# Kernel tuning notes

Hardware: AMD Instinct MI355X
Metric: run time of the kernel (lower is better)

The kernel has to match this reference:

```python
import jax, jax.numpy as jnp
import numpy as np
from jax.scipy.linalg import solve_triangular


def setup_inputs() -> dict:
    key = jax.random.key(0)
    k1, k2 = jax.random.split(key)
    # [K classes, N per class, D features] training embeddings
    src_seq = jax.random.normal(k1, (256, 64, 128), dtype=jnp.float32)
    # [M, D] vectors to project and pairwise-score (clustering inner loop)
    test = jax.random.normal(k2, (8192, 128), dtype=jnp.float32)
    return {"src_seq": src_seq, "test": test}


def _fit_model(src_seq):
    # Faithful port of compute_scatter_matrices + fit_model.
    # S_w, S_b are symmetric PSD, so solve(S_w,S_b) eig is replaced by the
    # equivalent (and differentiable) generalized symmetric eig via Cholesky
    # whitening; A_inverse and psi are invariant to eigvec scaling/order.
    K, N, D = src_seq.shape
    count = K * N
    mean_per_class = src_seq.mean(axis=1)            # [K, D]
    mean = src_seq.mean(axis=(0, 1))                 # [D]
    diff_w = src_seq - mean_per_class[:, None, :]    # [K, N, D]
    diff_b = mean_per_class - mean                   # [K, D]
    S_w = jnp.einsum('knd,kne->de', diff_w, diff_w) / count   # [D, D]
    S_b = (N * jnp.einsum('kd,ke->de', diff_b, diff_b)) / count

    L = jnp.linalg.cholesky(S_w)                     # S_w = L L^T
    # Msym = L^{-1} S_b L^{-T}
    tmp = solve_triangular(L, S_b, lower=True)
    Msym = solve_triangular(L, tmp.T, lower=True).T
    Msym = 0.5 * (Msym + Msym.T)
    evals, U = jnp.linalg.eigh(Msym)
    W = solve_triangular(L, U, lower=True, trans=1)  # W = L^{-T} U, eigvecs of S_w^{-1} S_b

    lambda_b = jnp.sum(W * (S_b @ W), axis=0)        # diag(W^T S_b W)
    lambda_w = jnp.sum(W * (S_w @ W), axis=0)        # diag(W^T S_w W)
    n = float(N)
    # A = W^{-T} diag(sqrt(n/(n-1) * lambda_w))  =>  A^{-1} = diag(1/sqrt(.)) W^T
    A_inverse = (1.0 / jnp.sqrt(n / (n - 1.0) * lambda_w))[:, None] * W.T
    psi = jnp.clip((n - 1.0) / n * (lambda_b / lambda_w) - 1.0 / n, 0.0)
    return A_inverse, mean, psi


def reference(src_seq, test):
    A_inverse, mean, psi = _fit_model(src_seq)
    # latent = A_inverse @ (x - mean), batched over rows
    latent = (test - mean) @ A_inverse.T             # [M, D]
    # Pairwise single-vector probability (calculate_probability_single),
    # vectorized over all (i, j) pairs, in log space:
    # log p(i,j) = -(v_i - v_j)^T diag(psi) (v_i - v_j)
    #             - 0.5 * (D*log(2*pi) + log(||psi||_F))
    D = latent.shape[1]
    q = jnp.sum(psi * latent * latent, axis=1)       # [M]
    G = (latent * psi) @ latent.T                    # [M, M]
    maha = q[:, None] + q[None, :] - 2.0 * G         # [M, M]
    log_div = 0.5 * (D * jnp.log(2.0 * jnp.pi) + jnp.log(jnp.linalg.norm(psi)))
    return -maha - log_div                           # [M, M] pairwise log-prob
```

## Files before the change

### kernel.cpp

```cpp
#include <hip/hip_runtime.h>
#include <math.h>


#define D 128
#define NCLS 256
#define NPC 64
#define MTEST 8192
#define COUNT (NCLS*NPC)

#define fMC    0
#define fMEAN  16384
#define fSCAL  16640
#define fMAT   32768
#define fSWRAW 442368
#define fPART  458752
#define fU     458752
#define fV     983040
#define fQ     1507328
#define fBBF   1515520

#define sP   0
#define sSB  1
#define sP2  2
#define sP3  3
#define sP4  4
#define sZ   5
#define sM1  6
#define sMm  7
#define sC2  8
#define sC4  9
#define sXH  10
#define sT2  11
#define sT3  12
#define sT4  13
#define sT5  14
#define sT10 15
#define sT15 16
#define sT20 17
#define sG0  18
#define sF   23
#define sA1  24

using short8 = __attribute__((ext_vector_type(8))) short;
using f32x4  = __attribute__((ext_vector_type(4))) float;

__device__ inline unsigned short f2bf(float f) {
  unsigned u = __float_as_uint(f);
  unsigned r = u + 0x7FFFu + ((u >> 16) & 1u);
  return (unsigned short)(r >> 16);
}
__device__ inline float bf2f(unsigned short h) {
  return __uint_as_float(((unsigned)h) << 16);
}
__device__ inline float valU(const unsigned short* m, int idx) {
  return bf2f(m[idx]) + bf2f(m[idx + 16384]);
}
__device__ inline void storeDual(unsigned short* m, int idx, float g) {
  unsigned short hb = f2bf(g);
  m[idx] = hb;
  m[16384 + idx] = f2bf(g - bf2f(hb));
}
__device__ inline unsigned short* MS(float* ws, int m) {
  return (unsigned short*)(ws + fMAT) + (size_t)m * 32768;
}
__device__ inline const unsigned short* MSc(const float* ws, int m) {
  return (const unsigned short*)(ws + fMAT) + (size_t)m * 32768;
}

__global__ __launch_bounds__(256) void k_gt_partial(const float* __restrict__ X, float* __restrict__ ws) {
  __shared__ unsigned short xt[128 * 256];
  int b = blockIdx.x, tid = threadIdx.x;
  const float* Xc = X + b * 256 * D;
  for (int idx = tid; idx < 256 * D; idx += 256) {
    int s = idx >> 7, d = idx & 127;
    unsigned byte = ((unsigned)(d * 512 + s * 2)) ^ (((unsigned)(d & 7)) << 4);
    *(unsigned short*)((char*)xt + byte) = f2bf(Xc[idx]);
  }
  {
    int d = tid & 127;
    for (int cc = (tid >> 7); cc < 4; cc += 2) {
      const float* p = Xc + cc * 64 * D + d;
      float s = 0.f;
      #pragma unroll
      for (int n = 0; n < 64; n++) s += p[n * D];
      ((unsigned short*)ws)[d * 256 + (b * 4 + cc)] = f2bf(s * (1.0f / 64.0f));
    }
  }
  __syncthreads();
  int w = tid >> 6, lane = tid & 63;
  int wr = (w >> 1) * 64, wc = (w & 1) * 64;
  f32x4 acc[4][4] = {};
  for (int ks = 0; ks < 8; ks++) {
    int kb = ks * 32 + (lane >> 4) * 8;
    short8 af[4];
    #pragma unroll
    for (int mt = 0; mt < 4; mt++) {
      int r = wr + mt * 16 + (lane & 15);
      unsigned byte = ((unsigned)(r * 512 + kb * 2)) ^ (((unsigned)(r & 7)) << 4);
      af[mt] = *(short8*)((char*)xt + byte);
    }
    #pragma unroll
    for (int nt = 0; nt < 4; nt++) {
      int c = wc + nt * 16 + (lane & 15);
      unsigned byte = ((unsigned)(c * 512 + kb * 2)) ^ (((unsigned)(c & 7)) << 4);
      short8 bfr = *(short8*)((char*)xt + byte);
      #pragma unroll
      for (int mt = 0; mt < 4; mt++)
        acc[mt][nt] = __builtin_amdgcn_mfma_f32_16x16x32_bf16(af[mt], bfr, acc[mt][nt], 0, 0, 0);
    }
  }
  float* outp = ws + fPART + b * 16384;
  #pragma unroll
  for (int mt = 0; mt < 4; mt++)
    #pragma unroll
    for (int nt = 0; nt < 4; nt++)
      #pragma unroll
      for (int r = 0; r < 4; r++) {
        int row = wr + mt * 16 + (lane >> 4) * 4 + r;
        int col = wc + nt * 16 + (lane & 15);
        outp[row * 128 + col] = acc[mt][nt][r];
      }
}

__global__ void k_reduce(float* __restrict__ ws) {
  int tid = threadIdx.x;
  int idx = blockIdx.x * 256 + tid;
  const float* part = ws + fPART;
  float s = 0.f;
  #pragma unroll 8
  for (int p = 0; p < 64; p++) s += part[p * 16384 + idx];
  ws[fSWRAW + idx] = s;
  if (blockIdx.x == 0 && tid < 128) {
    const unsigned short* McT = (const unsigned short*)ws;
    float m = 0.f;
    for (int k = 0; k < 256; k++) m += bf2f(McT[tid * 256 + k]);
    ws[fMEAN + tid] = m * (1.0f / 256.0f);
  }
}

__global__ __launch_bounds__(256) void k_sb(float* __restrict__ ws) {
  __shared__ float red[4];
  const unsigned short* Mc = (const unsigned short*)ws;
  const float* mv = ws + fMEAN;
  const float* swraw = ws + fSWRAW;
  unsigned short* SB = MS(ws, sSB);
  float* scal = ws + fSCAL;
  int tid = threadIdx.x, b = blockIdx.x;
  int w = tid >> 6, lane = tid & 63;
  int brow = b * 32, wcol = w * 32;
  f32x4 acc[2][2] = {};
  for (int ks = 0; ks < 8; ks++) {
    int kb = ks * 32 + (lane >> 4) * 8;
    short8 af[2], bfv[2];
    #pragma unroll
    for (int mt = 0; mt < 2; mt++) {
      int r = brow + mt * 16 + (lane & 15);
      af[mt] = *(const short8*)(Mc + r * 256 + kb);
    }
    #pragma unroll
    for (int nt = 0; nt < 2; nt++) {
      int c = wcol + nt * 16 + (lane & 15);
      bfv[nt] = *(const short8*)(Mc + c * 256 + kb);
    }
    #pragma unroll
    for (int mt = 0; mt < 2; mt++)
      #pragma unroll
      for (int nt = 0; nt < 2; nt++)
        acc[mt][nt] = __builtin_amdgcn_mfma_f32_16x16x32_bf16(af[mt], bfv[nt], acc[mt][nt], 0, 0, 0);
  }
  float tsum = 0.f;
  #pragma unroll
  for (int mt = 0; mt < 2; mt++)
    #pragma unroll
    for (int nt = 0; nt < 2; nt++)
      #pragma unroll
      for (int r = 0; r < 4; r++) {
        int row = brow + mt * 16 + (lane >> 4) * 4 + r;
        int col = wcol + nt * 16 + (lane & 15);
        int idx = row * 128 + col;
        float g = acc[mt][nt][r] * (1.0f / 256.0f) - mv[row] * mv[col];
        storeDual(SB, idx, g);
        if (row == col)
          tsum += swraw[row * 129] * (1.0f / COUNT) - g - mv[row] * mv[row];
      }
  #pragma unroll
  for (int off = 32; off > 0; off >>= 1) tsum += __shfl_down(tsum, off);
  if (lane == 0) red[w] = tsum;
  __syncthreads();
  if (tid == 0) scal[64 + b] = red[0] + red[1] + red[2] + red[3];
}

__global__ __launch_bounds__(256) void k_swfin(float* __restrict__ ws) {
  float* scal = ws + fSCAL;
  float inv_s = 128.0f / (scal[64] + scal[65] + scal[66] + scal[67]);
  const float* mv = ws + fMEAN;
  const float* swraw = ws + fSWRAW;
  const unsigned short* SB = MS(ws, sSB);
  unsigned short* P = MS(ws, sP);
  int gid = blockIdx.x * 256 + threadIdx.x;
  #pragma unroll
  for (int t = 0; t < 4; t++) {
    int idx = gid * 4 + t;
    int row = idx >> 7, col = idx & 127;
    float sb = valU(SB, idx);
    float s = (swraw[idx] * (1.0f / COUNT) - sb - mv[row] * mv[col]) * inv_s;
    storeDual(P, idx, s - ((row == col) ? 1.0f : 0.0f));
  }
  if (blockIdx.x == 0 && threadIdx.x == 0) {
    scal[1] = inv_s;
    scal[7] = 0.984375f * inv_s;
  }
}

__device__ __forceinline__ void mm_body(
    const unsigned short* __restrict__ A, const unsigned short* __restrict__ B,
    unsigned short* __restrict__ C, const unsigned short* __restrict__ E1,
    float alpha, const float* alpha_ptr, float beta, float delta,
    float* scal, int trace_slot, unsigned short* outBf, int b, float* red) {
  int tid = threadIdx.x;
  int w = tid >> 6, lane = tid & 63;
  int brow = b * 32, wcol = w * 32;
  f32x4 acc[2][2] = {};
  #pragma unroll
  for (int ks = 0; ks < 4; ks++) {
    int kb = ks * 32 + (lane >> 4) * 8;
    short8 ah[2], al[2], bh[2], bl[2];
    #pragma unroll
    for (int mt = 0; mt < 2; mt++) {
      int r = brow + mt * 16 + (lane & 15);
      ah[mt] = *(const short8*)(A + r * 128 + kb);
      al[mt] = *(const short8*)(A + 16384 + r * 128 + kb);
    }
    #pragma unroll
    for (int nt = 0; nt < 2; nt++) {
      int c = wcol + nt * 16 + (lane & 15);
      bh[nt] = *(const short8*)(B + c * 128 + kb);
      bl[nt] = *(const short8*)(B + 16384 + c * 128 + kb);
    }
    #pragma unroll
    for (int mt = 0; mt < 2; mt++)
      #pragma unroll
      for (int nt = 0; nt < 2; nt++) {
        f32x4 a0 = acc[mt][nt];
        a0 = __builtin_amdgcn_mfma_f32_16x16x32_bf16(ah[mt], bh[nt], a0, 0, 0, 0);
        a0 = __builtin_amdgcn_mfma_f32_16x16x32_bf16(al[mt], bh[nt], a0, 0, 0, 0);
        a0 = __builtin_amdgcn_mfma_f32_16x16x32_bf16(ah[mt], bl[nt], a0, 0, 0, 0);
        acc[mt][nt] = a0;
      }
  }
  float aeff = alpha * (alpha_ptr ? alpha_ptr[0] : 1.0f);
  float tsum = 0.0f;
  #pragma unroll
  for (int mt = 0; mt < 2; mt++)
    #pragma unroll
    for (int nt = 0; nt < 2; nt++)
      #pragma unroll
      for (int r = 0; r < 4; r++) {
        int row = brow + mt * 16 + (lane >> 4) * 4 + r;
        int col = wcol + nt * 16 + (lane & 15);
        int idx = row * 128 + col;
        float g = acc[mt][nt][r] * aeff;
        if (E1) g += beta * (bf2f(E1[idx]) + bf2f(E1[16384 + idx]));
        if (row == col) g += delta;
        if (outBf) outBf[idx] = f2bf(g);
        else storeDual(C, idx, g);
        tsum += g * g;
      }
  if (trace_slot >= 0) {
    #pragma unroll
    for (int off = 32; off > 0; off >>= 1) tsum += __shfl_down(tsum, off);
    if (lane == 0) red[w] = tsum;
    __syncthreads();
    if (tid == 0) scal[trace_slot + b] = red[0] + red[1] + red[2] + red[3];
  }
}

__global__ __launch_bounds__(256) void k_mm(
    const unsigned short* A, const unsigned short* B, unsigned short* C,
    const unsigned short* E1, float alpha, const float* alpha_ptr,
    float beta, float delta, float* scal, int trace_slot, unsigned short* outBf) {
  __shared__ float red[4];
  mm_body(A, B, C, E1, alpha, alpha_ptr, beta, delta, scal, trace_slot, outBf, blockIdx.x, red);
}

__global__ __launch_bounds__(256) void k_mm2(
    const unsigned short* A0, const unsigned short* B0, unsigned short* C0,
    const unsigned short* E0, float al0, float be0, float de0,
    const unsigned short* A1, const unsigned short* B1, unsigned short* C1,
    const unsigned short* E1, float al1, float be1, float de1,
    float* scal, int tslot1) {
  __shared__ float red[4];
  int b = blockIdx.x & 3;
  if (blockIdx.x < 4)
    mm_body(A0, B0, C0, E0, al0, nullptr, be0, de0, scal, -1, nullptr, b, red);
  else
    mm_body(A1, B1, C1, E1, al1, nullptr, be1, de1, scal, tslot1, nullptr, b, red);
}

__global__ __launch_bounds__(256) void k_p56z(float* __restrict__ ws) {
  __shared__ float cj[7];
  __shared__ float bt[7];
  float* scal = ws + fSCAL;
  const unsigned short *P = MSc(ws, sP), *P2 = MSc(ws, sP2),
    *P3 = MSc(ws, sP3), *P4 = MSc(ws, sP4);
  unsigned short* Z = MS(ws, sZ);
  int tid = threadIdx.x, b = blockIdx.x;
  float trP8 = scal[60] + scal[61] + scal[62] + scal[63];
  float a = 1.05f * sqrtf(sqrtf(sqrtf(fmaxf(trP8, 1e-30f))));
  a = fminf(a, 0.95f);
  if (tid < 7) {
    const float PI = 3.14159265358979f;
    float s = 0.f;
    for (int i = 0; i < 64; i++) {
      float th = (i + 0.5f) * (PI / 64.0f);
      float x = cosf(th);
      s += (1.0f / sqrtf(1.0f + a * x)) * cosf((float)tid * th);
    }
    cj[tid] = s * (2.0f / 64.0f);
  }
  __syncthreads();
  if (tid == 0) {
    float c0h = 0.5f * cj[0];
    float m0 = c0h - cj[2] + cj[4] - cj[6];
    float m1 = cj[1] - 3.0f * cj[3] + 5.0f * cj[5];
    float m2 = 2.0f * cj[2] - 8.0f * cj[4] + 18.0f * cj[6];
    float m3 = 4.0f * cj[3] - 20.0f * cj[5];
    float m4 = 8.0f * cj[4] - 48.0f * cj[6];
    float m5 = 16.0f * cj[5];
    float m6 = 32.0f * cj[6];
    float ia = 1.0f / a;
    float p = 1.f;
    bt[0] = m0;
    p *= ia; bt[1] = m1 * p;
    p *= ia; bt[2] = m2 * p;
    p *= ia; bt[3] = m3 * p;
    p *= ia; bt[4] = m4 * p;
    p *= ia; bt[5] = m5 * p;
    p *= ia; bt[6] = m6 * p;
  }
  __syncthreads();
  int w = tid >> 6, lane = tid & 63;
  int brow = b * 32, wcol = w * 32;
  f32x4 a5[2][2] = {}, a6[2][2] = {};
  #pragma unroll
  for (int ks = 0; ks < 4; ks++) {
    int kb = ks * 32 + (lane >> 4) * 8;
    short8 ah[2], al[2], b5h[2], b5l[2], b6h[2], b6l[2];
    #pragma unroll
    for (int mt = 0; mt < 2; mt++) {
      int r = brow + mt * 16 + (lane & 15);
      ah[mt] = *(const short8*)(P4 + r * 128 + kb);
      al[mt] = *(const short8*)(P4 + 16384 + r * 128 + kb);
    }
    #pragma unroll
    for (int nt = 0; nt < 2; nt++) {
      int c = wcol + nt * 16 + (lane & 15);
      b5h[nt] = *(const short8*)(P + c * 128 + kb);
      b5l[nt] = *(const short8*)(P + 16384 + c * 128 + kb);
      b6h[nt] = *(const short8*)(P2 + c * 128 + kb);
      b6l[nt] = *(const short8*)(P2 + 16384 + c * 128 + kb);
    }
    #pragma unroll
    for (int mt = 0; mt < 2; mt++)
      #pragma unroll
      for (int nt = 0; nt < 2; nt++) {
        f32x4 x5 = a5[mt][nt];
        x5 = __builtin_amdgcn_mfma_f32_16x16x32_bf16(ah[mt], b5h[nt], x5, 0, 0, 0);
        x5 = __builtin_amdgcn_mfma_f32_16x16x32_bf16(al[mt], b5h[nt], x5, 0, 0, 0);
        x5 = __builtin_amdgcn_mfma_f32_16x16x32_bf16(ah[mt], b5l[nt], x5, 0, 0, 0);
        a5[mt][nt] = x5;
        f32x4 x6 = a6[mt][nt];
        x6 = __builtin_amdgcn_mfma_f32_16x16x32_bf16(ah[mt], b6h[nt], x6, 0, 0, 0);
        x6 = __builtin_amdgcn_mfma_f32_16x16x32_bf16(al[mt], b6h[nt], x6, 0, 0, 0);
        x6 = __builtin_amdgcn_mfma_f32_16x16x32_bf16(ah[mt], b6l[nt], x6, 0, 0, 0);
        a6[mt][nt] = x6;
      }
  }
  #pragma unroll
  for (int mt = 0; mt < 2; mt++)
    #pragma unroll
    for (int nt = 0; nt < 2; nt++)
      #pragma unroll
      for (int r = 0; r < 4; r++) {
        int row = brow + mt * 16 + (lane >> 4) * 4 + r;
        int col = wcol + nt * 16 + (lane & 15);
        int idx = row * 128 + col;
        float dg = (row == col) ? 1.0f : 0.0f;
        float z = bt[0] * dg + bt[1] * valU(P, idx) + bt[2] * valU(P2, idx) +
                  bt[3] * valU(P3, idx) + bt[4] * valU(P4, idx) +
                  bt[5] * a5[mt][nt][r] + bt[6] * a6[mt][nt][r];
        storeDual(Z, idx, z);
      }
}

__device__ inline void interval_cs(const float* scal, float* c0o, float* iho) {
  float trM8 = scal[68] + scal[69] + scal[70] + scal[71];
  float Lam = 1.03f * sqrtf(sqrtf(sqrtf(fmaxf(trM8, 1e-37f))));
  float lo = -0.02f * Lam, hi = Lam;
  *c0o = 0.5f * (hi + lo);
  *iho = 1.0f / (0.5f * (hi - lo));
}

__global__ __launch_bounds__(256) void k_xh_t2(float* __restrict__ ws) {
  __shared__ float cs[2];
  float* scal = ws + fSCAL;
  if (threadIdx.x == 0) {
    float c0, ih;
    interval_cs(scal, &c0, &ih);
    cs[0] = c0; cs[1] = ih;
  }
  __syncthreads();
  float c0 = cs[0], ih = cs[1];
  float a2 = 2.0f * ih * ih, b2 = -4.0f * c0 * ih * ih, g2 = 2.0f * c0 * c0 * ih * ih - 1.0f;
  const unsigned short* Mm = MSc(ws, sMm);
  const unsigned short* C2 = MSc(ws, sC2);
  unsigned short* XH = MS(ws, sXH);
  unsigned short* T2 = MS(ws, sT2);
  int gid = blockIdx.x * 256 + threadIdx.x;
  #pragma unroll
  for (int t = 0; t < 4; t++) {
    int idx = gid * 4 + t;
    int row = idx >> 7, col = idx & 127;
    float m = valU(Mm, idx), c2v = valU(C2, idx);
    float dg = (row == col) ? 1.0f : 0.0f;
    storeDual(XH, idx, ih * m - ih * c0 * dg);
    storeDual(T2, idx, a2 * c2v + b2 * m + g2 * dg);
  }
}

__global__ __launch_bounds__(256) void k_t5g(float* __restrict__ ws) {
  __shared__ float red[4];
  __shared__ float cs[8];
  __shared__ float sat[25];
  __shared__ float sc[25];
  float* scal = ws + fSCAL;
  int tid = threadIdx.x;
  if (blockIdx.x < 4) {
    mm_body(MSc(ws, sT2), MSc(ws, sT3), MS(ws, sT5), MSc(ws, sXH),
            2.0f, nullptr, -1.0f, 0.0f, scal, -1, nullptr, blockIdx.x, red);
    return;
  }
  if (tid == 0) {
    float c0, ih;
    interval_cs(scal, &c0, &ih);
    float inv_s = scal[1];
    float t0 = (1.0f / 63.0f) / inv_s;
    float x0 = fminf(fmaxf((t0 - c0) * ih, -1.0f), 1.0f);
    cs[0] = acosf(x0); cs[1] = x0;
    cs[2] = 0.984375f * inv_s / ih;
  }
  __syncthreads();
  if (tid <= 24) {
    float th = cs[0], x0 = cs[1], SCc = cs[2];
    const float PI = 3.14159265358979f;
    float v;
    if (tid == 0) v = 0.5f * SCc * (2.0f / PI) * (sinf(th) - x0 * th);
    else if (tid == 1) v = SCc * (2.0f / PI) * (0.5f * th + 0.25f * sinf(2.0f * th) - x0 * sinf(th));
    else {
      float fj = (float)tid;
      v = SCc * (2.0f / PI) *
          (0.5f * (sinf((fj + 1.0f) * th) / (fj + 1.0f) + sinf((fj - 1.0f) * th) / (fj - 1.0f))
           - x0 * sinf(fj * th) / fj);
    }
    sat[tid] = v;
    sc[tid] = 0.f;
  }
  __syncthreads();
  if (tid == 0) {
    for (int j = 24; j >= 5; --j) {
      int k = j / 5, r = j - 5 * k;
      float aj = sat[j];
      if (r == 0) sc[k * 5] += aj;
      else { sc[k * 5 + r] += 2.0f * aj; sat[5 * k - r] -= aj; }
    }
    for (int r = 0; r < 5; r++) sc[r] += sat[r];
  }
  __syncthreads();
  const unsigned short* XH = MSc(ws, sXH);
  const unsigned short* T2 = MSc(ws, sT2);
  const unsigned short* T3 = MSc(ws, sT3);
  const unsigned short* T4 = MSc(ws, sT4);
  int bg = blockIdx.x - 4;
  int base = bg * 1024 + tid * 4;
  #pragma unroll
  for (int t = 0; t < 4; t++) {
    int idx = base + t;
    int row = idx >> 7, col = idx & 127;
    float dg = (row == col) ? 1.0f : 0.0f;
    float x1 = valU(XH, idx), x2 = valU(T2, idx), x3 = valU(T3, idx), x4 = valU(T4, idx);
    #pragma unroll
    for (int k = 0; k < 5; k++) {
      float g = sc[k * 5 + 0] * dg + sc[k * 5 + 1] * x1 + sc[k * 5 + 2] * x2 +
                sc[k * 5 + 3] * x3 + sc[k * 5 + 4] * x4;
      storeDual(MS(ws, sG0 + k), idx, g);
    }
  }
}

__global__ __launch_bounds__(256) void k_bigF(float* __restrict__ ws) {
  __shared__ float red[4];
  float* scal = ws + fSCAL;
  const unsigned short* As[4] = { MSc(ws, sT5), MSc(ws, sT10), MSc(ws, sT15), MSc(ws, sT20) };
  const unsigned short* Bs[4] = { MSc(ws, sG0 + 1), MSc(ws, sG0 + 2), MSc(ws, sG0 + 3), MSc(ws, sG0 + 4) };
  const unsigned short* G0 = MSc(ws, sG0);
  unsigned short* Fm = MS(ws, sF);
  int tid = threadIdx.x, b = blockIdx.x;
  int w = tid >> 6, lane = tid & 63;
  int brow = b * 32, wcol = w * 32;
  f32x4 acc[2][2] = {};
  for (int p = 0; p < 4; p++) {
    const unsigned short* A = As[p];
    const unsigned short* B = Bs[p];
    #pragma unroll
    for (int ks = 0; ks < 4; ks++) {
      int kb = ks * 32 + (lane >> 4) * 8;
      short8 ah[2], al[2], bh[2], bl[2];
      #pragma unroll
      for (int mt = 0; mt < 2; mt++) {
        int r = brow + mt * 16 + (lane & 15);
        ah[mt] = *(const short8*)(A + r * 128 + kb);
        al[mt] = *(const short8*)(A + 16384 + r * 128 + kb);
      }
      #pragma unroll
      for (int nt = 0; nt < 2; nt++) {
        int c = wcol + nt * 16 + (lane & 15);
        bh[nt] = *(const short8*)(B + c * 128 + kb);
        bl[nt] = *(const short8*)(B + 16384 + c * 128 + kb);
      }
      #pragma unroll
      for (int mt = 0; mt < 2; mt++)
        #pragma unroll
        for (int nt = 0; nt < 2; nt++) {
          f32x4 a0 = acc[mt][nt];
          a0 = __builtin_amdgcn_mfma_f32_16x16x32_bf16(ah[mt], bh[nt], a0, 0, 0, 0);
          a0 = __builtin_amdgcn_mfma_f32_16x16x32_bf16(al[mt], bh[nt], a0, 0, 0, 0);
          a0 = __builtin_amdgcn_mfma_f32_16x16x32_bf16(ah[mt], bl[nt], a0, 0, 0, 0);
          acc[mt][nt] = a0;
        }
    }
  }
  float tsum = 0.f;
  #pragma unroll
  for (int mt = 0; mt < 2; mt++)
    #pragma unroll
    for (int nt = 0; nt < 2; nt++)
      #pragma unroll
      for (int r = 0; r < 4; r++) {
        int row = brow + mt * 16 + (lane >> 4) * 4 + r;
        int col = wcol + nt * 16 + (lane & 15);
        int idx = row * 128 + col;
        float g = acc[mt][nt][r] + valU(G0, idx);
        storeDual(Fm, idx, g);
        tsum += g * g;
      }
  #pragma unroll
  for (int off = 32; off > 0; off >>= 1) tsum += __shfl_down(tsum, off);
  if (lane == 0) red[w] = tsum;
  __syncthreads();
  if (tid == 0) scal[72 + b] = red[0] + red[1] + red[2] + red[3];
}

__global__ __launch_bounds__(256) void k_latent(const float* __restrict__ test, float* __restrict__ ws) {
  __shared__ unsigned short vh[16384];
  __shared__ float qs[128];
  int blk = blockIdx.x, tid = threadIdx.x;
  if (blk == 0 && tid == 0) {
    float* scal = ws + fSCAL;
    float trF2 = fmaxf(scal[72] + scal[73] + scal[74] + scal[75], 1e-30f);
    scal[0] = 0.5f * (128.0f * 1.8378770664093453f + 0.5f * logf(trF2));
  }
  const float* tb = test + blk * 128 * D;
  unsigned short* Vbf = (unsigned short*)(ws + fV);
  if (tid < 128) qs[tid] = 0.f;
  for (int idx = tid; idx < 16384; idx += 256) {
    int r = idx >> 7, c = idx & 127;
    float v = tb[idx] - ws[fMEAN + c];
    unsigned short h = f2bf(v);
    unsigned byte = ((unsigned)(r * 256 + c * 2)) ^ (((unsigned)(r & 7)) << 4);
    *(unsigned short*)((char*)vh + byte) = h;
    Vbf[blk * 16384 + idx] = h;
  }
  __syncthreads();
  int w = tid >> 6, lane = tid & 63;
  int wr = (w >> 1) * 64, wc = (w & 1) * 64;
  const unsigned short* Bbf = (const unsigned short*)(ws + fBBF);
  f32x4 acc[4][4] = {};
  for (int ks = 0; ks < 4; ks++) {
    int kb = ks * 32 + (lane >> 4) * 8;
    short8 af[4], bfv[4];
    #pragma unroll
    for (int mt = 0; mt < 4; mt++) {
      int r = wr + mt * 16 + (lane & 15);
      unsigned byte = ((unsigned)(r * 256 + kb * 2)) ^ (((unsigned)(r & 7)) << 4);
      af[mt] = *(short8*)((char*)vh + byte);
    }
    #pragma unroll
    for (int nt = 0; nt < 4; nt++) {
      int c = wc + nt * 16 + (lane & 15);
      bfv[nt] = *(const short8*)(Bbf + c * 128 + kb);
    }
    #pragma unroll
    for (int mt = 0; mt < 4; mt++)
      #pragma unroll
      for (int nt = 0; nt < 4; nt++)
        acc[mt][nt] = __builtin_amdgcn_mfma_f32_16x16x32_bf16(af[mt], bfv[nt], acc[mt][nt], 0, 0, 0);
  }
  unsigned short* Ubf = (unsigned short*)(ws + fU);
  #pragma unroll
  for (int mt = 0; mt < 4; mt++)
    #pragma unroll
    for (int nt = 0; nt < 4; nt++)
      #pragma unroll
      for (int r = 0; r < 4; r++) {
        int row = wr + mt * 16 + (lane >> 4) * 4 + r;
        int col = wc + nt * 16 + (lane & 15);
        Ubf[(blk * 128 + row) * 128 + col] = f2bf(acc[mt][nt][r]);
      }
  #pragma unroll
  for (int mt = 0; mt < 4; mt++)
    #pragma unroll
    for (int r = 0; r < 4; r++) {
      int row = wr + mt * 16 + (lane >> 4) * 4 + r;
      float p = 0.f;
      #pragma unroll
      for (int nt = 0; nt < 4; nt++) {
        int col = wc + nt * 16 + (lane & 15);
        unsigned byte = ((unsigned)(row * 256 + col * 2)) ^ (((unsigned)(row & 7)) << 4);
        p += bf2f(f2bf(acc[mt][nt][r])) * bf2f(*(unsigned short*)((char*)vh + byte));
      }
      p += __shfl_xor(p, 1, 16);
      p += __shfl_xor(p, 2, 16);
      p += __shfl_xor(p, 4, 16);
      p += __shfl_xor(p, 8, 16);
      if ((lane & 15) == 0) atomicAdd(&qs[row], p);
    }
  __syncthreads();
  if (tid < 128) ws[fQ + blk * 128 + tid] = qs[tid];
}

__global__ __launch_bounds__(256) void k_pair(const float* __restrict__ ws, float* __restrict__ out) {
  __shared__ float qi[128];
  __shared__ float qj[128];
  __shared__ float sld;
  int bi = blockIdx.x, bj = blockIdx.y, tid = threadIdx.x;
  if (tid < 128) qi[tid] = ws[fQ + bi * 128 + tid];
  else qj[tid - 128] = ws[fQ + bj * 128 + (tid - 128)];
  if (tid == 0) sld = ws[fSCAL + 0];
  __syncthreads();
  int w = tid >> 6, lane = tid & 63;
  int wr = (w >> 1) * 64, wc = (w & 1) * 64;
  const unsigned short* Ubf = (const unsigned short*)(ws + fU);
  const unsigned short* Vbf = (const unsigned short*)(ws + fV);
  f32x4 acc[4][4] = {};
  for (int ks = 0; ks < 4; ks++) {
    int kb = ks * 32 + (lane >> 4) * 8;
    short8 af[4], bfv[4];
    #pragma unroll
    for (int mt = 0; mt < 4; mt++) {
      int r = bi * 128 + wr + mt * 16 + (lane & 15);
      af[mt] = *(const short8*)(Ubf + r * 128 + kb);
    }
    #pragma unroll
    for (int nt = 0; nt < 4; nt++) {
      int c = bj * 128 + wc + nt * 16 + (lane & 15);
      bfv[nt] = *(const short8*)(Vbf + c * 128 + kb);
    }
    #pragma unroll
    for (int mt = 0; mt < 4; mt++)
      #pragma unroll
      for (int nt = 0; nt < 4; nt++)
        acc[mt][nt] = __builtin_amdgcn_mfma_f32_16x16x32_bf16(af[mt], bfv[nt], acc[mt][nt], 0, 0, 0);
  }
  float ld = sld;
  #pragma unroll
  for (int mt = 0; mt < 4; mt++)
    #pragma unroll
    for (int nt = 0; nt < 4; nt++)
      #pragma unroll
      for (int r = 0; r < 4; r++) {
        int row = wr + mt * 16 + (lane >> 4) * 4 + r;
        int col = wc + nt * 16 + (lane & 15);
        float g = acc[mt][nt][r];
        out[(size_t)(bi * 128 + row) * MTEST + (bj * 128 + col)] =
          2.0f * g - qi[row] - qj[col] - ld;
      }
}

extern "C" void kernel_launch(void* const* d_in, const int* in_sizes, int n_in,
                              void* d_out, int out_size, void* d_ws, size_t ws_size,
                              hipStream_t stream) {
  (void)in_sizes; (void)n_in; (void)out_size; (void)ws_size;
  const float* X = (const float*)d_in[0];
  const float* test = (const float*)d_in[1];
  float* out = (float*)d_out;
  float* ws = (float*)d_ws;
  float* scal = ws + fSCAL;
  auto M = [&](int i) -> unsigned short* {
    return (unsigned short*)(ws + fMAT) + (size_t)i * 32768;
  };
  unsigned short* Bbf = (unsigned short*)(ws + fBBF);

  k_gt_partial<<<64, 256, 0, stream>>>(X, ws);
  k_reduce<<<64, 256, 0, stream>>>(ws);
  k_sb<<<4, 256, 0, stream>>>(ws);
  k_swfin<<<16, 256, 0, stream>>>(ws);
  k_mm<<<4, 256, 0, stream>>>(M(sP), M(sP), M(sP2), nullptr, 1.0f, nullptr, 0, 0, scal, -1, nullptr);
  k_mm2<<<8, 256, 0, stream>>>(M(sP2), M(sP), M(sP3), nullptr, 1.0f, 0, 0,
                               M(sP2), M(sP2), M(sP4), nullptr, 1.0f, 0, 0, scal, 60);
  k_p56z<<<4, 256, 0, stream>>>(ws);
  k_mm<<<4, 256, 0, stream>>>(M(sZ), M(sSB), M(sM1), nullptr, 1.0f, nullptr, 0, 0, scal, -1, nullptr);
  k_mm<<<4, 256, 0, stream>>>(M(sM1), M(sZ), M(sMm), nullptr, 1.0f, nullptr, 0, 0, scal, -1, nullptr);
  k_mm<<<4, 256, 0, stream>>>(M(sMm), M(sMm), M(sC2), nullptr, 1.0f, nullptr, 0, 0, scal, -1, nullptr);
  k_mm<<<4, 256, 0, stream>>>(M(sC2), M(sC2), M(sC4), nullptr, 1.0f, nullptr, 0, 0, scal, 68, nullptr);
  k_xh_t2<<<16, 256, 0, stream>>>(ws);
  k_mm2<<<8, 256, 0, stream>>>(M(sXH), M(sT2), M(sT3), M(sXH), 2.0f, -1.0f, 0,
                               M(sT2), M(sT2), M(sT4), nullptr, 2.0f, 0, -1.0f, scal, -1);
  k_t5g<<<20, 256, 0, stream>>>(ws);
  k_mm<<<4, 256, 0, stream>>>(M(sT5), M(sT5), M(sT10), nullptr, 2.0f, nullptr, 0, -1.0f, scal, -1, nullptr);
  k_mm2<<<8, 256, 0, stream>>>(M(sT10), M(sT5), M(sT15), M(sT5), 2.0f, -1.0f, 0,
                               M(sT10), M(sT10), M(sT20), nullptr, 2.0f, 0, -1.0f, scal, -1);
  k_bigF<<<4, 256, 0, stream>>>(ws);
  k_mm<<<4, 256, 0, stream>>>(M(sZ), M(sF), M(sA1), nullptr, 1.0f, nullptr, 0, 0, scal, -1, nullptr);
  k_mm<<<4, 256, 0, stream>>>(M(sA1), M(sZ), nullptr, nullptr, 1.0f, scal + 7, 0, 0, scal, -1, Bbf);
  k_latent<<<64, 256, 0, stream>>>(test, ws);
  k_pair<<<dim3(64, 64), 256, 0, stream>>>(ws, out);
}
```

Measured before the change: 277.8 us.

## Fuse matrix-function chain into fewer kernels with LDS-chained products

Cuts the serial chain of small 128x128 split-bf16 matmul launches from about 19 to about 13. It fuses S_b and P construction, computes the P^2/P^3/P^4 chain within a block using LDS-resident row tiles, and moves the test-minus-mean conversion into spare blocks of the powers kernel. It also lowers the polynomial/Chebyshev degrees (7-term to 5-term, T20 to T16 style), switches to 1024-thread blocks with one 16x16 tile per wave, and computes the S_w trace scale in the reduce kernel. The goal is less launch and dependency latency in the tiny sequential prologue before the large pairwise kernel. The lower approximation degree risks accuracy.

```diff
diff --git a/kernel.cpp b/kernel.cpp
--- a/kernel.cpp
+++ b/kernel.cpp
@@ -25,21 +25,17 @@
 #define sP3  3
 #define sP4  4
 #define sZ   5
-#define sM1  6
 #define sMm  7
 #define sC2  8
-#define sC4  9
 #define sXH  10
 #define sT2  11
 #define sT3  12
 #define sT4  13
-#define sT5  14
-#define sT10 15
-#define sT15 16
-#define sT20 17
+#define sT8  14
+#define sT12 15
+#define sT16 16
 #define sG0  18
 #define sF   23
-#define sA1  24
 
 using short8 = __attribute__((ext_vector_type(8))) short;
 using f32x4  = __attribute__((ext_vector_type(4))) float;
@@ -63,8 +59,52 @@
 __device__ inline unsigned short* MS(float* ws, int m) {
   return (unsigned short*)(ws + fMAT) + (size_t)m * 32768;
 }
-__device__ inline const unsigned short* MSc(const float* ws, int m) {
-  return (const unsigned short*)(ws + fMAT) + (size_t)m * 32768;
+__device__ inline short8 st8(const unsigned short* L, int rloc, int colk) {
+  unsigned u = ((unsigned)(rloc * 128 + colk)) ^ (((unsigned)(rloc & 7)) << 3);
+  return *(const short8*)(L + u);
+}
+__device__ inline float stValU(const unsigned short* L, int rloc, int col) {
+  unsigned u = ((unsigned)(rloc * 128 + col)) ^ (((unsigned)(rloc & 7)) << 3);
+  return bf2f(L[u]) + bf2f(L[4096 + u]);
+}
+__device__ inline void stPutDual(unsigned short* L, int rloc, int col, float g) {
+  unsigned u = ((unsigned)(rloc * 128 + col)) ^ (((unsigned)(rloc & 7)) << 3);
+  unsigned short hb = f2bf(g);
+  L[u] = hb;
+  L[4096 + u] = f2bf(g - bf2f(hb));
+}
+
+__device__ __forceinline__ f32x4 tile_AB(const unsigned short* __restrict__ A, int rA,
+                                         const unsigned short* __restrict__ B, int cB,
+                                         int lane, f32x4 acc) {
+  #pragma unroll
+  for (int ks = 0; ks < 4; ks++) {
+    int kb = ks * 32 + (lane >> 4) * 8;
+    short8 ah = *(const short8*)(A + rA * 128 + kb);
+    short8 al = *(const short8*)(A + 16384 + rA * 128 + kb);
+    short8 bh = *(const short8*)(B + cB * 128 + kb);
+    short8 bl = *(const short8*)(B + 16384 + cB * 128 + kb);
+    acc = __builtin_amdgcn_mfma_f32_16x16x32_bf16(ah, bh, acc, 0, 0, 0);
+    acc = __builtin_amdgcn_mfma_f32_16x16x32_bf16(al, bh, acc, 0, 0, 0);
+    acc = __builtin_amdgcn_mfma_f32_16x16x32_bf16(ah, bl, acc, 0, 0, 0);
+  }
+  return acc;
+}
+__device__ __forceinline__ f32x4 tile_LB(const unsigned short* __restrict__ L, int rloc,
+                                         const unsigned short* __restrict__ B, int cB,
+                                         int lane, f32x4 acc) {
+  #pragma unroll
+  for (int ks = 0; ks < 4; ks++) {
+    int kb = ks * 32 + (lane >> 4) * 8;
+    short8 ah = st8(L, rloc, kb);
+    short8 al = st8(L + 4096, rloc, kb);
+    short8 bh = *(const short8*)(B + cB * 128 + kb);
+    short8 bl = *(const short8*)(B + 16384 + cB * 128 + kb);
+    acc = __builtin_amdgcn_mfma_f32_16x16x32_bf16(ah, bh, acc, 0, 0, 0);
+    acc = __builtin_amdgcn_mfma_f32_16x16x32_bf16(al, bh, acc, 0, 0, 0);
+    acc = __builtin_amdgcn_mfma_f32_16x16x32_bf16(ah, bl, acc, 0, 0, 0);
+  }
+  return acc;
 }
 
 __global__ __launch_bounds__(256) void k_gt_partial(const float* __restrict__ X, float* __restrict__ ws) {
@@ -123,6 +163,7 @@
 }
 
 __global__ void k_reduce(float* __restrict__ ws) {
+  __shared__ float red2[4];
   int tid = threadIdx.x;
   int idx = blockIdx.x * 256 + tid;
   const float* part = ws + fPART;
@@ -136,179 +177,139 @@
     for (int k = 0; k < 256; k++) m += bf2f(McT[tid * 256 + k]);
     ws[fMEAN + tid] = m * (1.0f / 256.0f);
   }
-}
-
-__global__ __launch_bounds__(256) void k_sb(float* __restrict__ ws) {
-  __shared__ float red[4];
+  if (blockIdx.x == 1) {
+    float v = 0.f;
+    if (tid < 128) {
+      float gdd = 0.f;
+      for (int p = 0; p < 64; p++) gdd += part[p * 16384 + tid * 129];
+      const unsigned short* McT = (const unsigned short*)ws;
+      float nrm = 0.f;
+      for (int k = 0; k < 256; k++) { float x = bf2f(McT[tid * 256 + k]); nrm += x * x; }
+      v = gdd * (1.0f / COUNT) - nrm * (1.0f / 256.0f);
+    }
+    #pragma unroll
+    for (int off = 32; off > 0; off >>= 1) v += __shfl_down(v, off);
+    if ((tid & 63) == 0) red2[tid >> 6] = v;
+    __syncthreads();
+    if (tid == 0) {
+      float inv_s = 128.0f / (red2[0] + red2[1] + red2[2] + red2[3]);
+      ws[fSCAL + 1] = inv_s;
+      ws[fSCAL + 7] = 0.984375f * inv_s;
+    }
+  }
+}
+
+__global__ __launch_bounds__(1024) void k_sbp(float* __restrict__ ws) {
   const unsigned short* Mc = (const unsigned short*)ws;
   const float* mv = ws + fMEAN;
   const float* swraw = ws + fSWRAW;
+  float inv_s = ws[fSCAL + 1];
   unsigned short* SB = MS(ws, sSB);
+  unsigned short* P = MS(ws, sP);
+  int tid = threadIdx.x, b = blockIdx.x;
+  int w = tid >> 6, lane = tid & 63;
+  int wr = (w & 1) * 16, wc = (w >> 1) * 16;
+  int brow = b * 32;
+  f32x4 acc = {};
+  for (int ks = 0; ks < 8; ks++) {
+    int kb = ks * 32 + (lane >> 4) * 8;
+    short8 af = *(const short8*)(Mc + (brow + wr + (lane & 15)) * 256 + kb);
+    short8 bf = *(const short8*)(Mc + (wc + (lane & 15)) * 256 + kb);
+    acc = __builtin_amdgcn_mfma_f32_16x16x32_bf16(af, bf, acc, 0, 0, 0);
+  }
+  #pragma unroll
+  for (int r = 0; r < 4; r++) {
+    int row = brow + wr + (lane >> 4) * 4 + r;
+    int col = wc + (lane & 15);
+    int idx = row * 128 + col;
+    float g = acc[r] * (1.0f / 256.0f) - mv[row] * mv[col];
+    storeDual(SB, idx, g);
+    float s = (swraw[idx] * (1.0f / COUNT) - g - mv[row] * mv[col]) * inv_s;
+    storeDual(P, idx, s - ((row == col) ? 1.0f : 0.0f));
+  }
+}
+
+__global__ __launch_bounds__(1024) void k_pows(const float* __restrict__ test, float* __restrict__ ws) {
+  __shared__ unsigned short sA[8192];
+  __shared__ unsigned short sB[8192];
+  __shared__ float red[16];
   float* scal = ws + fSCAL;
   int tid = threadIdx.x, b = blockIdx.x;
-  int w = tid >> 6, lane = tid & 63;
-  int brow = b * 32, wcol = w * 32;
-  f32x4 acc[2][2] = {};
-  for (int ks = 0; ks < 8; ks++) {
-    int kb = ks * 32 + (lane >> 4) * 8;
-    short8 af[2], bfv[2];
-    #pragma unroll
-    for (int mt = 0; mt < 2; mt++) {
-      int r = brow + mt * 16 + (lane & 15);
-      af[mt] = *(const short8*)(Mc + r * 256 + kb);
-    }
-    #pragma unroll
-    for (int nt = 0; nt < 2; nt++) {
-      int c = wcol + nt * 16 + (lane & 15);
-      bfv[nt] = *(const short8*)(Mc + c * 256 + kb);
-    }
-    #pragma unroll
-    for (int mt = 0; mt < 2; mt++)
-      #pragma unroll
-      for (int nt = 0; nt < 2; nt++)
-        acc[mt][nt] = __builtin_amdgcn_mfma_f32_16x16x32_bf16(af[mt], bfv[nt], acc[mt][nt], 0, 0, 0);
-  }
+  if (b >= 4) {
+    unsigned short* Vbf = (unsigned short*)(ws + fV);
+    const float* mv = ws + fMEAN;
+    int base = (b - 4) * 32768;
+    #pragma unroll 4
+    for (int k = 0; k < 32; k++) {
+      int idx = base + k * 1024 + tid;
+      Vbf[idx] = f2bf(test[idx] - mv[idx & 127]);
+    }
+    return;
+  }
+  const unsigned short* P = MS(ws, sP);
+  unsigned short* P2 = MS(ws, sP2);
+  unsigned short* P3 = MS(ws, sP3);
+  unsigned short* P4 = MS(ws, sP4);
+  int w = tid >> 6, lane = tid & 63;
+  int wr = (w & 1) * 16, wc = (w >> 1) * 16;
+  int brow = b * 32;
   float tsum = 0.f;
-  #pragma unroll
-  for (int mt = 0; mt < 2; mt++)
-    #pragma unroll
-    for (int nt = 0; nt < 2; nt++)
-      #pragma unroll
-      for (int r = 0; r < 4; r++) {
-        int row = brow + mt * 16 + (lane >> 4) * 4 + r;
-        int col = wcol + nt * 16 + (lane & 15);
-        int idx = row * 128 + col;
-        float g = acc[mt][nt][r] * (1.0f / 256.0f) - mv[row] * mv[col];
-        storeDual(SB, idx, g);
-        if (row == col)
-          tsum += swraw[row * 129] * (1.0f / COUNT) - g - mv[row] * mv[row];
-      }
+  {
+    f32x4 acc = {};
+    acc = tile_AB(P, brow + wr + (lane & 15), P, wc + (lane & 15), lane, acc);
+    #pragma unroll
+    for (int r = 0; r < 4; r++) {
+      int rloc = wr + (lane >> 4) * 4 + r;
+      int col = wc + (lane & 15);
+      float g = acc[r];
+      stPutDual(sA, rloc, col, g);
+      storeDual(P2, (brow + rloc) * 128 + col, g);
+      tsum += g * g;
+    }
+  }
   #pragma unroll
   for (int off = 32; off > 0; off >>= 1) tsum += __shfl_down(tsum, off);
   if (lane == 0) red[w] = tsum;
   __syncthreads();
-  if (tid == 0) scal[64 + b] = red[0] + red[1] + red[2] + red[3];
-}
-
-__global__ __launch_bounds__(256) void k_swfin(float* __restrict__ ws) {
+  if (tid == 0) {
+    float s = 0.f;
+    #pragma unroll
+    for (int i = 0; i < 16; i++) s += red[i];
+    scal[60 + b] = s;
+  }
+  {
+    f32x4 acc = {};
+    acc = tile_LB(sA, wr + (lane & 15), P, wc + (lane & 15), lane, acc);
+    #pragma unroll
+    for (int r = 0; r < 4; r++) {
+      int rloc = wr + (lane >> 4) * 4 + r;
+      int col = wc + (lane & 15);
+      stPutDual(sB, rloc, col, acc[r]);
+      storeDual(P3, (brow + rloc) * 128 + col, acc[r]);
+    }
+  }
+  __syncthreads();
+  {
+    f32x4 acc = {};
+    acc = tile_LB(sB, wr + (lane & 15), P, wc + (lane & 15), lane, acc);
+    #pragma unroll
+    for (int r = 0; r < 4; r++) {
+      int rloc = wr + (lane >> 4) * 4 + r;
+      int col = wc + (lane & 15);
+      storeDual(P4, (brow + rloc) * 128 + col, acc[r]);
+    }
+  }
+}
+
+__global__ __launch_bounds__(256) void k_z(float* __restrict__ ws) {
+  __shared__ float cj[5];
+  __shared__ float bt[5];
   float* scal = ws + fSCAL;
-  float inv_s = 128.0f / (scal[64] + scal[65] + scal[66] + scal[67]);
-  const float* mv = ws + fMEAN;
-  const float* swraw = ws + fSWRAW;
-  const unsigned short* SB = MS(ws, sSB);
-  unsigned short* P = MS(ws, sP);
-  int gid = blockIdx.x * 256 + threadIdx.x;
-  #pragma unroll
-  for (int t = 0; t < 4; t++) {
-    int idx = gid * 4 + t;
-    int row = idx >> 7, col = idx & 127;
-    float sb = valU(SB, idx);
-    float s = (swraw[idx] * (1.0f / COUNT) - sb - mv[row] * mv[col]) * inv_s;
-    storeDual(P, idx, s - ((row == col) ? 1.0f : 0.0f));
-  }
-  if (blockIdx.x == 0 && threadIdx.x == 0) {
-    scal[1] = inv_s;
-    scal[7] = 0.984375f * inv_s;
-  }
-}
-
-__device__ __forceinline__ void mm_body(
-    const unsigned short* __restrict__ A, const unsigned short* __restrict__ B,
-    unsigned short* __restrict__ C, const unsigned short* __restrict__ E1,
-    float alpha, const float* alpha_ptr, float beta, float delta,
-    float* scal, int trace_slot, unsigned short* outBf, int b, float* red) {
   int tid = threadIdx.x;
-  int w = tid >> 6, lane = tid & 63;
-  int brow = b * 32, wcol = w * 32;
-  f32x4 acc[2][2] = {};
-  #pragma unroll
-  for (int ks = 0; ks < 4; ks++) {
-    int kb = ks * 32 + (lane >> 4) * 8;
-    short8 ah[2], al[2], bh[2], bl[2];
-    #pragma unroll
-    for (int mt = 0; mt < 2; mt++) {
-      int r = brow + mt * 16 + (lane & 15);
-      ah[mt] = *(const short8*)(A + r * 128 + kb);
-      al[mt] = *(const short8*)(A + 16384 + r * 128 + kb);
-    }
-    #pragma unroll
-    for (int nt = 0; nt < 2; nt++) {
-      int c = wcol + nt * 16 + (lane & 15);
-      bh[nt] = *(const short8*)(B + c * 128 + kb);
-      bl[nt] = *(const short8*)(B + 16384 + c * 128 + kb);
-    }
-    #pragma unroll
-    for (int mt = 0; mt < 2; mt++)
-      #pragma unroll
-      for (int nt = 0; nt < 2; nt++) {
-        f32x4 a0 = acc[mt][nt];
-        a0 = __builtin_amdgcn_mfma_f32_16x16x32_bf16(ah[mt], bh[nt], a0, 0, 0, 0);
-        a0 = __builtin_amdgcn_mfma_f32_16x16x32_bf16(al[mt], bh[nt], a0, 0, 0, 0);
-        a0 = __builtin_amdgcn_mfma_f32_16x16x32_bf16(ah[mt], bl[nt], a0, 0, 0, 0);
-        acc[mt][nt] = a0;
-      }
-  }
-  float aeff = alpha * (alpha_ptr ? alpha_ptr[0] : 1.0f);
-  float tsum = 0.0f;
-  #pragma unroll
-  for (int mt = 0; mt < 2; mt++)
-    #pragma unroll
-    for (int nt = 0; nt < 2; nt++)
-      #pragma unroll
-      for (int r = 0; r < 4; r++) {
-        int row = brow + mt * 16 + (lane >> 4) * 4 + r;
-        int col = wcol + nt * 16 + (lane & 15);
-        int idx = row * 128 + col;
-        float g = acc[mt][nt][r] * aeff;
-        if (E1) g += beta * (bf2f(E1[idx]) + bf2f(E1[16384 + idx]));
-        if (row == col) g += delta;
-        if (outBf) outBf[idx] = f2bf(g);
-        else storeDual(C, idx, g);
-        tsum += g * g;
-      }
-  if (trace_slot >= 0) {
-    #pragma unroll
-    for (int off = 32; off > 0; off >>= 1) tsum += __shfl_down(tsum, off);
-    if (lane == 0) red[w] = tsum;
-    __syncthreads();
-    if (tid == 0) scal[trace_slot + b] = red[0] + red[1] + red[2] + red[3];
-  }
-}
-
-__global__ __launch_bounds__(256) void k_mm(
-    const unsigned short* A, const unsigned short* B, unsigned short* C,
-    const unsigned short* E1, float alpha, const float* alpha_ptr,
-    float beta, float delta, float* scal, int trace_slot, unsigned short* outBf) {
-  __shared__ float red[4];
-  mm_body(A, B, C, E1, alpha, alpha_ptr, beta, delta, scal, trace_slot, outBf, blockIdx.x, red);
-}
-
-__global__ __launch_bounds__(256) void k_mm2(
-    const unsigned short* A0, const unsigned short* B0, unsigned short* C0,
-    const unsigned short* E0, float al0, float be0, float de0,
-    const unsigned short* A1, const unsigned short* B1, unsigned short* C1,
-    const unsigned short* E1, float al1, float be1, float de1,
-    float* scal, int tslot1) {
-  __shared__ float red[4];
-  int b = blockIdx.x & 3;
-  if (blockIdx.x < 4)
-    mm_body(A0, B0, C0, E0, al0, nullptr, be0, de0, scal, -1, nullptr, b, red);
-  else
-    mm_body(A1, B1, C1, E1, al1, nullptr, be1, de1, scal, tslot1, nullptr, b, red);
-}
-
-__global__ __launch_bounds__(256) void k_p56z(float* __restrict__ ws) {
-  __shared__ float cj[7];
-  __shared__ float bt[7];
-  float* scal = ws + fSCAL;
-  const unsigned short *P = MSc(ws, sP), *P2 = MSc(ws, sP2),
-    *P3 = MSc(ws, sP3), *P4 = MSc(ws, sP4);
-  unsigned short* Z = MS(ws, sZ);
-  int tid = threadIdx.x, b = blockIdx.x;
-  float trP8 = scal[60] + scal[61] + scal[62] + scal[63];
-  float a = 1.05f * sqrtf(sqrtf(sqrtf(fmaxf(trP8, 1e-30f))));
-  a = fminf(a, 0.95f);
-  if (tid < 7) {
+  float trP4 = scal[60] + scal[61] + scal[62] + scal[63];
+  float a = 1.05f * sqrtf(sqrtf(fmaxf(trP4, 1e-30f)));
+  a = fminf(fmaxf(a, 1e-3f), 0.95f);
+  if (tid < 5) {
     const float PI = 3.14159265358979f;
     float s = 0.f;
     for (int i = 0; i < 64; i++) {
@@ -321,81 +322,97 @@
   __syncthreads();
   if (tid == 0) {
     float c0h = 0.5f * cj[0];
-    float m0 = c0h - cj[2] + cj[4] - cj[6];
-    float m1 = cj[1] - 3.0f * cj[3] + 5.0f * cj[5];
-    float m2 = 2.0f * cj[2] - 8.0f * cj[4] + 18.0f * cj[6];
-    float m3 = 4.0f * cj[3] - 20.0f * cj[5];
-    float m4 = 8.0f * cj[4] - 48.0f * cj[6];
-    float m5 = 16.0f * cj[5];
-    float m6 = 32.0f * cj[6];
-    float ia = 1.0f / a;
-    float p = 1.f;
+    float m0 = c0h - cj[2] + cj[4];
+    float m1 = cj[1] - 3.0f * cj[3];
+    float m2 = 2.0f * cj[2] - 8.0f * cj[4];
+    float m3 = 4.0f * cj[3];
+    float m4 = 8.0f * cj[4];
+    float ia = 1.0f / a, p = 1.f;
     bt[0] = m0;
     p *= ia; bt[1] = m1 * p;
     p *= ia; bt[2] = m2 * p;
     p *= ia; bt[3] = m3 * p;
     p *= ia; bt[4] = m4 * p;
-    p *= ia; bt[5] = m5 * p;
-    p *= ia; bt[6] = m6 * p;
-  }
-  __syncthreads();
-  int w = tid >> 6, lane = tid & 63;
-  int brow = b * 32, wcol = w * 32;
-  f32x4 a5[2][2] = {}, a6[2][2] = {};
-  #pragma unroll
-  for (int ks = 0; ks < 4; ks++) {
-    int kb = ks * 32 + (lane >> 4) * 8;
-    short8 ah[2], al[2], b5h[2], b5l[2], b6h[2], b6l[2];
-    #pragma unroll
-    for (int mt = 0; mt < 2; mt++) {
-      int r = brow + mt * 16 + (lane & 15);
-      ah[mt] = *(const short8*)(P4 + r * 128 + kb);
-      al[mt] = *(const short8*)(P4 + 16384 + r * 128 + kb);
-    }
-    #pragma unroll
-    for (int nt = 0; nt < 2; nt++) {
-      int c = wcol + nt * 16 + (lane & 15);
-      b5h[nt] = *(const short8*)(P + c * 128 + kb);
-      b5l[nt] = *(const short8*)(P + 16384 + c * 128 + kb);
-      b6h[nt] = *(const short8*)(P2 + c * 128 + kb);
-      b6l[nt] = *(const short8*)(P2 + 16384 + c * 128 + kb);
-    }
-    #pragma unroll
-    for (int mt = 0; mt < 2; mt++)
-      #pragma unroll
-      for (int nt = 0; nt < 2; nt++) {
-        f32x4 x5 = a5[mt][nt];
-        x5 = __builtin_amdgcn_mfma_f32_16x16x32_bf16(ah[mt], b5h[nt], x5, 0, 0, 0);
-        x5 = __builtin_amdgcn_mfma_f32_16x16x32_bf16(al[mt], b5h[nt], x5, 0, 0, 0);
-        x5 = __builtin_amdgcn_mfma_f32_16x16x32_bf16(ah[mt], b5l[nt], x5, 0, 0, 0);
-        a5[mt][nt] = x5;
-        f32x4 x6 = a6[mt][nt];
-        x6 = __builtin_amdgcn_mfma_f32_16x16x32_bf16(ah[mt], b6h[nt], x6, 0, 0, 0);
-        x6 = __builtin_amdgcn_mfma_f32_16x16x32_bf16(al[mt], b6h[nt], x6, 0, 0, 0);
-        x6 = __builtin_amdgcn_mfma_f32_16x16x32_bf16(ah[mt], b6l[nt], x6, 0, 0, 0);
-        a6[mt][nt] = x6;
-      }
-  }
-  #pragma unroll
-  for (int mt = 0; mt < 2; mt++)
-    #pragma unroll
-    for (int nt = 0; nt < 2; nt++)
-      #pragma unroll
-      for (int r = 0; r < 4; r++) {
-        int row = brow + mt * 16 + (lane >> 4) * 4 + r;
-        int col = wcol + nt * 16 + (lane & 15);
-        int idx = row * 128 + col;
-        float dg = (row == col) ? 1.0f : 0.0f;
-        float z = bt[0] * dg + bt[1] * valU(P, idx) + bt[2] * valU(P2, idx) +
-                  bt[3] * valU(P3, idx) + bt[4] * valU(P4, idx) +
-                  bt[5] * a5[mt][nt][r] + bt[6] * a6[mt][nt][r];
-        storeDual(Z, idx, z);
-      }
+  }
+  __syncthreads();
+  const unsigned short *P = MS(ws, sP), *P2 = MS(ws, sP2),
+    *P3 = MS(ws, sP3), *P4 = MS(ws, sP4);
+  unsigned short* Z = MS(ws, sZ);
+  float b0 = bt[0], b1 = bt[1], b2 = bt[2], b3 = bt[3], b4 = bt[4];
+  int gid = blockIdx.x * 256 + tid;
+  #pragma unroll
+  for (int t = 0; t < 4; t++) {
+    int idx = gid * 4 + t;
+    int row = idx >> 7, col = idx & 127;
+    float dg = (row == col) ? 1.0f : 0.0f;
+    float z = b0 * dg + b1 * valU(P, idx) + b2 * valU(P2, idx) +
+              b3 * valU(P3, idx) + b4 * valU(P4, idx);
+    storeDual(Z, idx, z);
+  }
+}
+
+__global__ __launch_bounds__(1024) void k_m(float* __restrict__ ws) {
+  __shared__ unsigned short sA[8192];
+  const unsigned short* Z = MS(ws, sZ);
+  const unsigned short* SB = MS(ws, sSB);
+  unsigned short* Mm = MS(ws, sMm);
+  int tid = threadIdx.x, b = blockIdx.x;
+  int w = tid >> 6, lane = tid & 63;
+  int wr = (w & 1) * 16, wc = (w >> 1) * 16;
+  int brow = b * 32;
+  {
+    f32x4 acc = {};
+    acc = tile_AB(Z, brow + wr + (lane & 15), SB, wc + (lane & 15), lane, acc);
+    #pragma unroll
+    for (int r = 0; r < 4; r++)
+      stPutDual(sA, wr + (lane >> 4) * 4 + r, wc + (lane & 15), acc[r]);
+  }
+  __syncthreads();
+  {
+    f32x4 acc = {};
+    acc = tile_LB(sA, wr + (lane & 15), Z, wc + (lane & 15), lane, acc);
+    #pragma unroll
+    for (int r = 0; r < 4; r++) {
+      int rloc = wr + (lane >> 4) * 4 + r;
+      storeDual(Mm, (brow + rloc) * 128 + wc + (lane & 15), acc[r]);
+    }
+  }
+}
+
+__global__ __launch_bounds__(1024) void k_c2(float* __restrict__ ws) {
+  __shared__ float red[16];
+  float* scal = ws + fSCAL;
+  const unsigned short* Mm = MS(ws, sMm);
+  unsigned short* C2 = MS(ws, sC2);
+  int tid = threadIdx.x, b = blockIdx.x;
+  int w = tid >> 6, lane = tid & 63;
+  int wr = (w & 1) * 16, wc = (w >> 1) * 16;
+  int brow = b * 32;
+  f32x4 acc = {};
+  acc = tile_AB(Mm, brow + wr + (lane & 15), Mm, wc + (lane & 15), lane, acc);
+  float tsum = 0.f;
+  #pragma unroll
+  for (int r = 0; r < 4; r++) {
+    int rloc = wr + (lane >> 4) * 4 + r;
+    float g = acc[r];
+    storeDual(C2, (brow + rloc) * 128 + wc + (lane & 15), g);
+    tsum += g * g;
+  }
+  #pragma unroll
+  for (int off = 32; off > 0; off >>= 1) tsum += __shfl_down(tsum, off);
+  if (lane == 0) red[w] = tsum;
+  __syncthreads();
+  if (tid == 0) {
+    float s = 0.f;
+    #pragma unroll
+    for (int i = 0; i < 16; i++) s += red[i];
+    scal[68 + b] = s;
+  }
 }
 
 __device__ inline void interval_cs(const float* scal, float* c0o, float* iho) {
-  float trM8 = scal[68] + scal[69] + scal[70] + scal[71];
-  float Lam = 1.03f * sqrtf(sqrtf(sqrtf(fmaxf(trM8, 1e-37f))));
+  float trM4 = scal[68] + scal[69] + scal[70] + scal[71];
+  float Lam = 1.03f * sqrtf(sqrtf(fmaxf(trM4, 1e-37f)));
   float lo = -0.02f * Lam, hi = Lam;
   *c0o = 0.5f * (hi + lo);
   *iho = 1.0f / (0.5f * (hi - lo));
@@ -412,8 +429,8 @@
   __syncthreads();
   float c0 = cs[0], ih = cs[1];
   float a2 = 2.0f * ih * ih, b2 = -4.0f * c0 * ih * ih, g2 = 2.0f * c0 * c0 * ih * ih - 1.0f;
-  const unsigned short* Mm = MSc(ws, sMm);
-  const unsigned short* C2 = MSc(ws, sC2);
+  const unsigned short* Mm = MS(ws, sMm);
+  const unsigned short* C2 = MS(ws, sC2);
   unsigned short* XH = MS(ws, sXH);
   unsigned short* T2 = MS(ws, sT2);
   int gid = blockIdx.x * 256 + threadIdx.x;
@@ -428,16 +445,90 @@
   }
 }
 
-__global__ __launch_bounds__(256) void k_t5g(float* __restrict__ ws) {
-  __shared__ float red[4];
-  __shared__ float cs[8];
-  __shared__ float sat[25];
-  __shared__ float sc[25];
+__global__ __launch_bounds__(1024) void k_t34(float* __restrict__ ws) {
+  const unsigned short* XH = MS(ws, sXH);
+  const unsigned short* T2 = MS(ws, sT2);
+  int tid = threadIdx.x;
+  int w = tid >> 6, lane = tid & 63;
+  int wr = (w & 1) * 16, wc = (w >> 1) * 16;
+  if (blockIdx.x < 4) {
+    int brow = blockIdx.x * 32;
+    f32x4 acc = {};
+    acc = tile_AB(XH, brow + wr + (lane & 15), T2, wc + (lane & 15), lane, acc);
+    unsigned short* T3 = MS(ws, sT3);
+    #pragma unroll
+    for (int r = 0; r < 4; r++) {
+      int idx = (brow + wr + (lane >> 4) * 4 + r) * 128 + wc + (lane & 15);
+      storeDual(T3, idx, 2.0f * acc[r] - valU(XH, idx));
+    }
+  } else {
+    int brow = (blockIdx.x - 4) * 32;
+    f32x4 acc = {};
+    acc = tile_AB(T2, brow + wr + (lane & 15), T2, wc + (lane & 15), lane, acc);
+    unsigned short* T4 = MS(ws, sT4);
+    #pragma unroll
+    for (int r = 0; r < 4; r++) {
+      int row = brow + wr + (lane >> 4) * 4 + r;
+      int col = wc + (lane & 15);
+      storeDual(T4, row * 128 + col, 2.0f * acc[r] - ((row == col) ? 1.0f : 0.0f));
+    }
+  }
+}
+
+__global__ __launch_bounds__(1024) void k_t8g(float* __restrict__ ws) {
+  __shared__ unsigned short sA[8192];
+  __shared__ unsigned short sB[8192];
+  __shared__ float cs[4];
+  __shared__ float sat[20];
+  __shared__ float sc[20];
   float* scal = ws + fSCAL;
   int tid = threadIdx.x;
+  const unsigned short* T4 = MS(ws, sT4);
   if (blockIdx.x < 4) {
-    mm_body(MSc(ws, sT2), MSc(ws, sT3), MS(ws, sT5), MSc(ws, sXH),
-            2.0f, nullptr, -1.0f, 0.0f, scal, -1, nullptr, blockIdx.x, red);
+    int b = blockIdx.x, brow = b * 32;
+    int w = tid >> 6, lane = tid & 63;
+    int wr = (w & 1) * 16, wc = (w >> 1) * 16;
+    unsigned short* T8 = MS(ws, sT8);
+    unsigned short* T12 = MS(ws, sT12);
+    unsigned short* T16 = MS(ws, sT16);
+    {
+      f32x4 acc = {};
+      acc = tile_AB(T4, brow + wr + (lane & 15), T4, wc + (lane & 15), lane, acc);
+      #pragma unroll
+      for (int r = 0; r < 4; r++) {
+        int rloc = wr + (lane >> 4) * 4 + r;
+        int row = brow + rloc, col = wc + (lane & 15);
+        float g = 2.0f * acc[r] - ((row == col) ? 1.0f : 0.0f);
+        stPutDual(sA, rloc, col, g);
+        storeDual(T8, row * 128 + col, g);
+      }
+    }
+    __syncthreads();
+    {
+      f32x4 acc = {};
+      acc = tile_LB(sA, wr + (lane & 15), T4, wc + (lane & 15), lane, acc);
+      #pragma unroll
+      for (int r = 0; r < 4; r++) {
+        int rloc = wr + (lane >> 4) * 4 + r;
+        int col = wc + (lane & 15);
+        int idx = (brow + rloc) * 128 + col;
+        float g = 2.0f * acc[r] - valU(T4, idx);
+        stPutDual(sB, rloc, col, g);
+        storeDual(T12, idx, g);
+      }
+    }
+    __syncthreads();
+    {
+      f32x4 acc = {};
+      acc = tile_LB(sB, wr + (lane & 15), T4, wc + (lane & 15), lane, acc);
+      #pragma unroll
+      for (int r = 0; r < 4; r++) {
+        int rloc = wr + (lane >> 4) * 4 + r;
+        int col = wc + (lane & 15);
+        float g = 2.0f * acc[r] - stValU(sA, rloc, col);
+        storeDual(T16, (brow + rloc) * 128 + col, g);
+      }
+    }
     return;
   }
   if (tid == 0) {
@@ -450,7 +541,7 @@
     cs[2] = 0.984375f * inv_s / ih;
   }
   __syncthreads();
-  if (tid <= 24) {
+  if (tid <= 19) {
     float th = cs[0], x0 = cs[1], SCc = cs[2];
     const float PI = 3.14159265358979f;
     float v;
@@ -467,100 +558,98 @@
   }
   __syncthreads();
   if (tid == 0) {
-    for (int j = 24; j >= 5; --j) {
-      int k = j / 5, r = j - 5 * k;
+    for (int j = 19; j >= 4; --j) {
+      int k = j >> 2, r = j & 3;
       float aj = sat[j];
-      if (r == 0) sc[k * 5] += aj;
-      else { sc[k * 5 + r] += 2.0f * aj; sat[5 * k - r] -= aj; }
-    }
-    for (int r = 0; r < 5; r++) sc[r] += sat[r];
-  }
-  __syncthreads();
-  const unsigned short* XH = MSc(ws, sXH);
-  const unsigned short* T2 = MSc(ws, sT2);
-  const unsigned short* T3 = MSc(ws, sT3);
-  const unsigned short* T4 = MSc(ws, sT4);
-  int bg = blockIdx.x - 4;
-  int base = bg * 1024 + tid * 4;
-  #pragma unroll
-  for (int t = 0; t < 4; t++) {
-    int idx = base + t;
+      if (r == 0) sc[k * 4] += aj;
+      else { sc[k * 4 + r] += 2.0f * aj; sat[4 * k - r] -= aj; }
+    }
+    for (int r = 0; r < 4; r++) sc[r] += sat[r];
+  }
+  __syncthreads();
+  const unsigned short* XH = MS(ws, sXH);
+  const unsigned short* T2 = MS(ws, sT2);
+  const unsigned short* T3 = MS(ws, sT3);
+  int idx = (blockIdx.x - 4) * 1024 + tid;
+  {
     int row = idx >> 7, col = idx & 127;
     float dg = (row == col) ? 1.0f : 0.0f;
-    float x1 = valU(XH, idx), x2 = valU(T2, idx), x3 = valU(T3, idx), x4 = valU(T4, idx);
+    float x1 = valU(XH, idx), x2 = valU(T2, idx), x3 = valU(T3, idx);
     #pragma unroll
     for (int k = 0; k < 5; k++) {
-      float g = sc[k * 5 + 0] * dg + sc[k * 5 + 1] * x1 + sc[k * 5 + 2] * x2 +
-                sc[k * 5 + 3] * x3 + sc[k * 5 + 4] * x4;
+      float g = sc[k * 4 + 0] * dg + sc[k * 4 + 1] * x1 + sc[k * 4 + 2] * x2 +
+                sc[k * 4 + 3] * x3;
       storeDual(MS(ws, sG0 + k), idx, g);
     }
   }
 }
 
-__global__ __launch_bounds__(256) void k_bigF(float* __restrict__ ws) {
-  __shared__ float red[4];
+__global__ __launch_bounds__(1024) void k_bigF(float* __restrict__ ws) {
+  __shared__ float red[16];
   float* scal = ws + fSCAL;
-  const unsigned short* As[4] = { MSc(ws, sT5), MSc(ws, sT10), MSc(ws, sT15), MSc(ws, sT20) };
-  const unsigned short* Bs[4] = { MSc(ws, sG0 + 1), MSc(ws, sG0 + 2), MSc(ws, sG0 + 3), MSc(ws, sG0 + 4) };
-  const unsigned short* G0 = MSc(ws, sG0);
+  const unsigned short* G0 = MS(ws, sG0);
   unsigned short* Fm = MS(ws, sF);
   int tid = threadIdx.x, b = blockIdx.x;
   int w = tid >> 6, lane = tid & 63;
-  int brow = b * 32, wcol = w * 32;
-  f32x4 acc[2][2] = {};
-  for (int p = 0; p < 4; p++) {
-    const unsigned short* A = As[p];
-    const unsigned short* B = Bs[p];
-    #pragma unroll
-    for (int ks = 0; ks < 4; ks++) {
-      int kb = ks * 32 + (lane >> 4) * 8;
-      short8 ah[2], al[2], bh[2], bl[2];
-      #pragma unroll
-      for (int mt = 0; mt < 2; mt++) {
-        int r = brow + mt * 16 + (lane & 15);
-        ah[mt] = *(const short8*)(A + r * 128 + kb);
-        al[mt] = *(const short8*)(A + 16384 + r * 128 + kb);
-      }
-      #pragma unroll
-      for (int nt = 0; nt < 2; nt++) {
-        int c = wcol + nt * 16 + (lane & 15);
-        bh[nt] = *(const short8*)(B + c * 128 + kb);
-        bl[nt] = *(const short8*)(B + 16384 + c * 128 + kb);
-      }
-      #pragma unroll
-      for (int mt = 0; mt < 2; mt++)
-        #pragma unroll
-        for (int nt = 0; nt < 2; nt++) {
-          f32x4 a0 = acc[mt][nt];
-          a0 = __builtin_amdgcn_mfma_f32_16x16x32_bf16(ah[mt], bh[nt], a0, 0, 0, 0);
-          a0 = __builtin_amdgcn_mfma_f32_16x16x32_bf16(al[mt], bh[nt], a0, 0, 0, 0);
-          a0 = __builtin_amdgcn_mfma_f32_16x16x32_bf16(ah[mt], bl[nt], a0, 0, 0, 0);
-          acc[mt][nt] = a0;
-        }
-    }
-  }
+  int wr = (w & 1) * 16, wc = (w >> 1) * 16;
+  int brow = b * 32;
+  int rA = brow + wr + (lane & 15), cB = wc + (lane & 15);
+  f32x4 acc = {};
+  acc = tile_AB(MS(ws, sT4), rA, MS(ws, sG0 + 1), cB, lane, acc);
+  acc = tile_AB(MS(ws, sT8), rA, MS(ws, sG0 + 2), cB, lane, acc);
+  acc = tile_AB(MS(ws, sT12), rA, MS(ws, sG0 + 3), cB, lane, acc);
+  acc = tile_AB(MS(ws, sT16), rA, MS(ws, sG0 + 4), cB, lane, acc);
   float tsum = 0.f;
   #pragma unroll
-  for (int mt = 0; mt < 2; mt++)
-    #pragma unroll
-    for (int nt = 0; nt < 2; nt++)
-      #pragma unroll
-      for (int r = 0; r < 4; r++) {
-        int row = brow + mt * 16 + (lane >> 4) * 4 + r;
-        int col = wcol + nt * 16 + (lane & 15);
-        int idx = row * 128 + col;
-        float g = acc[mt][nt][r] + valU(G0, idx);
-        storeDual(Fm, idx, g);
-        tsum += g * g;
-      }
+  for (int r = 0; r < 4; r++) {
+    int rloc = wr + (lane >> 4) * 4 + r;
+    int idx = (brow + rloc) * 128 + wc + (lane & 15);
+    float g = acc[r] + valU(G0, idx);
+    storeDual(Fm, idx, g);
+    tsum += g * g;
+  }
   #pragma unroll
   for (int off = 32; off > 0; off >>= 1) tsum += __shfl_down(tsum, off);
   if (lane == 0) red[w] = tsum;
   __syncthreads();
-  if (tid == 0) scal[72 + b] = red[0] + red[1] + red[2] + red[3];
-}
-
-__global__ __launch_bounds__(256) void k_latent(const float* __restrict__ test, float* __restrict__ ws) {
+  if (tid == 0) {
+    float s = 0.f;
+    #pragma unroll
+    for (int i = 0; i < 16; i++) s += red[i];
+    scal[72 + b] = s;
+  }
+}
+
+__global__ __launch_bounds__(1024) void k_b(float* __restrict__ ws) {
+  __shared__ unsigned short sA[8192];
+  const unsigned short* Z = MS(ws, sZ);
+  const unsigned short* Fm = MS(ws, sF);
+  unsigned short* Bbf = (unsigned short*)(ws + fBBF);
+  float aeff = ws[fSCAL + 7];
+  int tid = threadIdx.x, b = blockIdx.x;
+  int w = tid >> 6, lane = tid & 63;
+  int wr = (w & 1) * 16, wc = (w >> 1) * 16;
+  int brow = b * 32;
+  {
+    f32x4 acc = {};
+    acc = tile_AB(Z, brow + wr + (lane & 15), Fm, wc + (lane & 15), lane, acc);
+    #pragma unroll
+    for (int r = 0; r < 4; r++)
+      stPutDual(sA, wr + (lane >> 4) * 4 + r, wc + (lane & 15), acc[r]);
+  }
+  __syncthreads();
+  {
+    f32x4 acc = {};
+    acc = tile_LB(sA, wr + (lane & 15), Z, wc + (lane & 15), lane, acc);
+    #pragma unroll
+    for (int r = 0; r < 4; r++) {
+      int rloc = wr + (lane >> 4) * 4 + r;
+      Bbf[(brow + rloc) * 128 + wc + (lane & 15)] = f2bf(acc[r] * aeff);
+    }
+  }
+}
+
+__global__ __launch_bounds__(256) void k_latent(float* __restrict__ ws) {
   __shared__ unsigned short vh[16384];
   __shared__ float qs[128];
   int blk = blockIdx.x, tid = threadIdx.x;
@@ -569,16 +658,13 @@
     float trF2 = fmaxf(scal[72] + scal[73] + scal[74] + scal[75], 1e-30f);
     scal[0] = 0.5f * (128.0f * 1.8378770664093453f + 0.5f * logf(trF2));
   }
-  const float* tb = test + blk * 128 * D;
-  unsigned short* Vbf = (unsigned short*)(ws + fV);
+  const unsigned short* Vbf = (const unsigned short*)(ws + fV);
   if (tid < 128) qs[tid] = 0.f;
   for (int idx = tid; idx < 16384; idx += 256) {
     int r = idx >> 7, c = idx & 127;
-    float v = tb[idx] - ws[fMEAN + c];
-    unsigned short h = f2bf(v);
+    unsigned short h = Vbf[blk * 16384 + idx];
     unsigned byte = ((unsigned)(r * 256 + c * 2)) ^ (((unsigned)(r & 7)) << 4);
     *(unsigned short*)((char*)vh + byte) = h;
-    Vbf[blk * 16384 + idx] = h;
   }
   __syncthreads();
   int w = tid >> 6, lane = tid & 63;
@@ -694,34 +780,19 @@
   const float* test = (const float*)d_in[1];
   float* out = (float*)d_out;
   float* ws = (float*)d_ws;
-  float* scal = ws + fSCAL;
-  auto M = [&](int i) -> unsigned short* {
-    return (unsigned short*)(ws + fMAT) + (size_t)i * 32768;
-  };
-  unsigned short* Bbf = (unsigned short*)(ws + fBBF);
 
   k_gt_partial<<<64, 256, 0, stream>>>(X, ws);
   k_reduce<<<64, 256, 0, stream>>>(ws);
-  k_sb<<<4, 256, 0, stream>>>(ws);
-  k_swfin<<<16, 256, 0, stream>>>(ws);
-  k_mm<<<4, 256, 0, stream>>>(M(sP), M(sP), M(sP2), nullptr, 1.0f, nullptr, 0, 0, scal, -1, nullptr);
-  k_mm2<<<8, 256, 0, stream>>>(M(sP2), M(sP), M(sP3), nullptr, 1.0f, 0, 0,
-                               M(sP2), M(sP2), M(sP4), nullptr, 1.0f, 0, 0, scal, 60);
-  k_p56z<<<4, 256, 0, stream>>>(ws);
-  k_mm<<<4, 256, 0, stream>>>(M(sZ), M(sSB), M(sM1), nullptr, 1.0f, nullptr, 0, 0, scal, -1, nullptr);
-  k_mm<<<4, 256, 0, stream>>>(M(sM1), M(sZ), M(sMm), nullptr, 1.0f, nullptr, 0, 0, scal, -1, nullptr);
-  k_mm<<<4, 256, 0, stream>>>(M(sMm), M(sMm), M(sC2), nullptr, 1.0f, nullptr, 0, 0, scal, -1, nullptr);
-  k_mm<<<4, 256, 0, stream>>>(M(sC2), M(sC2), M(sC4), nullptr, 1.0f, nullptr, 0, 0, scal, 68, nullptr);
+  k_sbp<<<4, 1024, 0, stream>>>(ws);
+  k_pows<<<36, 1024, 0, stream>>>(test, ws);
+  k_z<<<16, 256, 0, stream>>>(ws);
+  k_m<<<4, 1024, 0, stream>>>(ws);
+  k_c2<<<4, 1024, 0, stream>>>(ws);
   k_xh_t2<<<16, 256, 0, stream>>>(ws);
-  k_mm2<<<8, 256, 0, stream>>>(M(sXH), M(sT2), M(sT3), M(sXH), 2.0f, -1.0f, 0,
-                               M(sT2), M(sT2), M(sT4), nullptr, 2.0f, 0, -1.0f, scal, -1);
-  k_t5g<<<20, 256, 0, stream>>>(ws);
-  k_mm<<<4, 256, 0, stream>>>(M(sT5), M(sT5), M(sT10), nullptr, 2.0f, nullptr, 0, -1.0f, scal, -1, nullptr);
-  k_mm2<<<8, 256, 0, stream>>>(M(sT10), M(sT5), M(sT15), M(sT5), 2.0f, -1.0f, 0,
-                               M(sT10), M(sT10), M(sT20), nullptr, 2.0f, 0, -1.0f, scal, -1);
-  k_bigF<<<4, 256, 0, stream>>>(ws);
-  k_mm<<<4, 256, 0, stream>>>(M(sZ), M(sF), M(sA1), nullptr, 1.0f, nullptr, 0, 0, scal, -1, nullptr);
-  k_mm<<<4, 256, 0, stream>>>(M(sA1), M(sZ), nullptr, nullptr, 1.0f, scal + 7, 0, 0, scal, -1, Bbf);
-  k_latent<<<64, 256, 0, stream>>>(test, ws);
+  k_t34<<<8, 1024, 0, stream>>>(ws);
+  k_t8g<<<20, 1024, 0, stream>>>(ws);
+  k_bigF<<<4, 1024, 0, stream>>>(ws);
+  k_b<<<4, 1024, 0, stream>>>(ws);
+  k_latent<<<64, 256, 0, stream>>>(ws);
   k_pair<<<dim3(64, 64), 256, 0, stream>>>(ws, out);
 }
```

Result: faster. 271.3 us (-2.3%).
